# Performance work log

Hardware: AMD Instinct MI355X
Metric: run time of the kernel (lower is better)

The kernel has to match this reference:

```python
import jax, jax.numpy as jnp
import numpy as np

B, S, HID, H = 8, 128, 256, 4
DH = HID // H
FF = 4 * HID


def setup_inputs() -> dict:
    key = jax.random.key(0)
    ks = jax.random.split(key, 16)
    n = lambda i, shape: jax.random.normal(ks[i], shape, dtype=jnp.float32) * 0.02
    z = lambda shape: jnp.zeros(shape, dtype=jnp.float32)
    return dict(
        x=jax.random.normal(ks[0], (B, S, HID), dtype=jnp.float32),
        attention_mask=jnp.zeros((B, 1, S, S), dtype=jnp.float32),
        Wq=n(1, (HID, HID)), bq=z((HID,)),
        Wk=n(2, (HID, HID)), bk=z((HID,)),
        Wv=n(3, (HID, HID)), bv=z((HID,)),
        order_w=n(4, (2 * DH,)), order_b=z(()),
        dist_w=n(5, (2 * DH,)), dist_b=z(()),
        scalar=jax.random.normal(ks[6], (1,), dtype=jnp.float32),
        AWq=n(7, (HID, HID)), Abq=z((HID,)),
        AWk=n(8, (HID, HID)), Abk=z((HID,)),
        Wd=n(9, (HID, HID)), bd=z((HID,)),
        g1=jnp.ones((HID,), jnp.float32), beta1=z((HID,)),
        W1=n(10, (HID, FF)), b1=z((FF,)),
        W2=n(11, (FF, HID)), b2=z((HID,)),
        g2=jnp.ones((HID,), jnp.float32), beta2=z((HID,)),
    )


def _ln(t, g, b, eps=1e-12):
    m = t.mean(-1, keepdims=True)
    v = ((t - m) ** 2).mean(-1, keepdims=True)
    return (t - m) / jnp.sqrt(v + eps) * g + b


def _heads(t):
    # [B,S,HID] -> [B,H,S,DH]
    return t.reshape(B, S, H, DH).transpose(0, 2, 1, 3)


def reference(x, attention_mask, Wq, bq, Wk, bk, Wv, bv, order_w, order_b,
              dist_w, dist_b, scalar, AWq, Abq, AWk, Abk, Wd, bd,
              g1, beta1, W1, b1, W2, b2, g2, beta2):
    inv = 1.0 / jnp.sqrt(jnp.float32(DH))
    q = x @ Wq + bq
    k = x @ Wk + bk
    v = x @ Wv + bv
    qh, kh, vh = _heads(q), _heads(k), _heads(v)
    scores = jnp.einsum('bhqd,bhkd->bhqk', qh, kh)  # [B,H,S,S]

    # order/distance affines on concat(q_i, k_j): Linear(2*DH,1) decomposes into
    # per-token projections summed via broadcast (same math, no [B,H,S,S,2*DH] tensor)
    pr_order = jax.nn.sigmoid((qh @ order_w[:DH])[..., :, None]
                              + (kh @ order_w[DH:])[..., None, :] + order_b)
    gd_order = jnp.triu(jnp.ones((S, S), jnp.float32), k=1)
    err_order = (jnp.log(pr_order + 1e-24) * gd_order
                 + jnp.log(1.0 - pr_order + 1e-24) * (1.0 - gd_order))

    idx = jnp.arange(S)
    gd_dist = jnp.log(jnp.abs(idx[None, :] - idx[:, None]).astype(jnp.float32) + 1.0)
    pr_dist = ((qh @ dist_w[:DH])[..., :, None]
               + (kh @ dist_w[DH:])[..., None, :] + dist_b)
    err_dist = -jnp.square(gd_dist - pr_dist) * jnp.square(scalar[0]) * 0.5

    rich_scores = scores + err_order + err_dist
    softm = lambda s: jax.nn.softmax(s * inv + attention_mask, axis=-1)
    rich_probs = softm(rich_scores)
    origin_probs = softm(scores)

    # rich/calibrated combine ('fixed'): softmax(origin + 0.5 * rich)
    combined = jax.nn.softmax(origin_probs + 0.5 * rich_probs, axis=-1)

    # two-level attack attention on transformed mixed q/k
    aq, ak = _heads(q @ AWq + Abq), _heads(k @ AWk + Abk)
    attack_probs = softm(jnp.einsum('bhqd,bhkd->bhqk', aq, ak))
    final_probs = jax.nn.softmax(combined + 0.5 * attack_probs, axis=-1)

    ctx = jnp.einsum('bhqk,bhkd->bhqd', final_probs, vh)
    ctx = ctx.transpose(0, 2, 1, 3).reshape(B, S, HID)
    h = _ln(ctx @ Wd + bd + x, g1, beta1)
    f = jax.nn.gelu(h @ W1 + b1, approximate=False) @ W2 + b2
    return _ln(f + h, g2, beta2)
```

## Files before the change

### kernel.cpp

```cpp
#include <hip/hip_runtime.h>
#include <hip/hip_bf16.h>
#include <math.h>

#define B_  8
#define S_  128
#define HID_ 256
#define H_  4
#define DH_ 64
#define FF_ 1024
#define M_  (B_ * S_)

typedef _Float16 half_t;
typedef __attribute__((ext_vector_type(8))) _Float16 half8;
typedef __attribute__((ext_vector_type(4))) float floatx4;

enum { EP_F32 = 0, EP_F16 = 1, EP_F16B = 2, EP_GELU = 3, EP_PROJ = 4 };

__device__ __forceinline__ floatx4 mfma16(half8 a, half8 b, floatx4 c) {
    return __builtin_amdgcn_mfma_f32_16x16x32_f16(a, b, c, 0, 0, 0);
}

__device__ __forceinline__ float wred_sum(float v) {
#pragma unroll
    for (int o = 32; o >= 1; o >>= 1) v += __shfl_xor(v, o, 64);
    return v;
}
__device__ __forceinline__ float block_sum_256(float v, float* s4, int tid) {
    v = wred_sum(v);
    __syncthreads();
    if ((tid & 63) == 0) s4[tid >> 6] = v;
    __syncthreads();
    return s4[0] + s4[1] + s4[2] + s4[3];
}
__device__ __forceinline__ float qred_sum(float v) {
#pragma unroll
    for (int o = 1; o < 16; o <<= 1) v += __shfl_xor(v, o, 64);
    return v;
}
__device__ __forceinline__ void sm8(float (&v)[8]) {
    float s = 0.f;
#pragma unroll
    for (int j = 0; j < 8; ++j) { v[j] = __expf(v[j]); s += v[j]; }
    s = qred_sum(s);
    float r = 1.f / s;
#pragma unroll
    for (int j = 0; j < 8; ++j) v[j] *= r;
}

template<int EPI>
__device__ __forceinline__ void mgemm(
    const half_t* __restrict__ A, int ldA,
    const half_t* __restrict__ Bt, int ldB,
    int kLen, int m0, int n0,
    const float* __restrict__ bias,
    float* __restrict__ Cf, half_t* __restrict__ Ch, int ldC,
    const float* __restrict__ pw1, const float* __restrict__ pw2,
    float* __restrict__ po1, float* __restrict__ po2, int hsel)
{
    __shared__ half8 Asf[2][4][64];
    __shared__ half8 Bsf[2][4][64];

    const int tid = threadIdx.x;
    const int w = tid >> 6, l = tid & 63;
    const int sr = tid >> 2;
    const int sq = tid & 3;
    const int sdst = (sr & 15) | (sq << 4);
    const int smt = sr >> 4;
    const half_t* Ap = A + (size_t)(m0 + sr) * ldA + sq * 8;
    const half_t* Bp = Bt + (size_t)(n0 + sr) * ldB + sq * 8;

    half8 ra, rb;
    auto fetch = [&](int t) {
        ra = *(const half8*)(Ap + t * 32);
        rb = *(const half8*)(Bp + t * 32);
    };
    auto commit = [&](int buf) {
        Asf[buf][smt][sdst] = ra;
        Bsf[buf][smt][sdst] = rb;
    };

    floatx4 zero = {0.f, 0.f, 0.f, 0.f};
    floatx4 acc[4] = {zero, zero, zero, zero};
    const int kt = kLen >> 5;

    fetch(0);
    commit(0);
    __syncthreads();
    for (int t = 0; t < kt; ++t) {
        const bool more = (t + 1 < kt);
        if (more) fetch(t + 1);
        const int buf = t & 1;
        half8 a = Asf[buf][w][l];
        acc[0] = mfma16(a, Bsf[buf][0][l], acc[0]);
        acc[1] = mfma16(a, Bsf[buf][1][l], acc[1]);
        acc[2] = mfma16(a, Bsf[buf][2][l], acc[2]);
        acc[3] = mfma16(a, Bsf[buf][3][l], acc[3]);
        if (more) {
            commit((t + 1) & 1);
            __syncthreads();
        }
    }

    const int quad = l >> 4, lc = l & 15;
    const int rowb = m0 + w * 16 + quad * 4;
    float bvv[4] = {0.f, 0.f, 0.f, 0.f};
    if (EPI >= EP_F16B) {
#pragma unroll
        for (int nt = 0; nt < 4; ++nt) bvv[nt] = bias[n0 + nt * 16 + lc];
    }
    float pw1v[4], pw2v[4];
    if (EPI == EP_PROJ) {
#pragma unroll
        for (int nt = 0; nt < 4; ++nt) {
            pw1v[nt] = pw1[nt * 16 + lc];
            pw2v[nt] = pw2[nt * 16 + lc];
        }
    }
#pragma unroll
    for (int rr = 0; rr < 4; ++rr) {
        float ov[4];
#pragma unroll
        for (int nt = 0; nt < 4; ++nt) {
            float o = acc[nt][rr];
            if (EPI >= EP_F16B) o += bvv[nt];
            if (EPI == EP_GELU) o = 0.5f * o * (1.f + erff(o * 0.70710678118654752f));
            ov[nt] = o;
            const size_t ci = (size_t)(rowb + rr) * ldC + n0 + nt * 16 + lc;
            if (EPI == EP_F32) Cf[ci] = o;
            else Ch[ci] = (half_t)o;
        }
        if (EPI == EP_PROJ) {
            float po = ov[0] * pw1v[0] + ov[1] * pw1v[1] + ov[2] * pw1v[2] + ov[3] * pw1v[3];
            float pd = ov[0] * pw2v[0] + ov[1] * pw2v[1] + ov[2] * pw2v[2] + ov[3] * pw2v[3];
#pragma unroll
            for (int off = 1; off < 16; off <<= 1) {
                po += __shfl_xor(po, off, 64);
                pd += __shfl_xor(pd, off, 64);
            }
            if (lc == 0) {
                const int m = rowb + rr;
                const int idx = ((m >> 7) * H_ + hsel) * S_ + (m & 127);
                po1[idx] = po;
                po2[idx] = pd;
            }
        }
    }
}

__global__ __launch_bounds__(256) void prep_kernel(
    const float* __restrict__ x,
    const float* __restrict__ Wq, const float* __restrict__ Wk,
    const float* __restrict__ Wv, const float* __restrict__ Wd,
    const float* __restrict__ AWq, const float* __restrict__ AWk,
    const float* __restrict__ W1, const float* __restrict__ W2,
    half_t* __restrict__ x16, half_t* __restrict__ Wq16n, half_t* __restrict__ Wk16n,
    half_t* __restrict__ WqT, half_t* __restrict__ WkT, half_t* __restrict__ WvT,
    half_t* __restrict__ WdT, half_t* __restrict__ AWqT, half_t* __restrict__ AWkT,
    half_t* __restrict__ W1T, half_t* __restrict__ W2T)
{
    const int z = blockIdx.z, bx = blockIdx.x, by = blockIdx.y;
    const int tid = threadIdx.x;
    if (z < 3) {
        const float* src = (z == 0) ? x : (z == 1) ? Wq : Wk;
        half_t* dst = (z == 0) ? x16 : (z == 1) ? Wq16n : Wk16n;
        const int total = (z == 0) ? M_ * HID_ : HID_ * HID_;
        const int bid = by * 16 + bx;
        if (bid * 1024 < total) {
            const int base = bid * 1024 + tid * 4;
            float4 vv = *(const float4*)(src + base);
            dst[base + 0] = (half_t)vv.x;
            dst[base + 1] = (half_t)vv.y;
            dst[base + 2] = (half_t)vv.z;
            dst[base + 3] = (half_t)vv.w;
        }
        return;
    }
    const float* src; half_t* dst; int K, N, k0, n0;
    if (z <= 8) {
        const float* ins[6] = {Wq, Wk, Wv, Wd, AWq, AWk};
        half_t* outs[6] = {WqT, WkT, WvT, WdT, AWqT, AWkT};
        src = ins[z - 3]; dst = outs[z - 3];
        K = 256; N = 256; k0 = bx * 64; n0 = by * 64;
        if (bx >= 4 || by >= 4) return;
    } else if (z == 9) {
        src = W1; dst = W1T; K = 256; N = 1024;
        k0 = bx * 64; n0 = by * 64;
        if (bx >= 4) return;
    } else {
        src = W2; dst = W2T; K = 1024; N = 256;
        k0 = by * 64; n0 = bx * 64;
        if (bx >= 4) return;
    }
    __shared__ half_t tl[64][72];
    const int r = tid >> 2, c0 = (tid & 3) * 16;
#pragma unroll 4
    for (int i = 0; i < 16; ++i)
        tl[c0 + i][r] = (half_t)src[(size_t)(k0 + r) * N + n0 + c0 + i];
    __syncthreads();
#pragma unroll 4
    for (int i = 0; i < 16; ++i)
        dst[(size_t)(n0 + r) * K + k0 + c0 + i] = tl[r][c0 + i];
}

__global__ __launch_bounds__(256) void compose_mfma(
    const half_t* __restrict__ AWqT, const half_t* __restrict__ AWkT,
    const half_t* __restrict__ Wq16n, const half_t* __restrict__ Wk16n,
    const float* __restrict__ AWq, const float* __restrict__ AWk,
    const float* __restrict__ bq, const float* __restrict__ bk,
    const float* __restrict__ Abq, const float* __restrict__ Abk,
    half_t* __restrict__ WcqT, half_t* __restrict__ WckT,
    float* __restrict__ bcq, float* __restrict__ bck)
{
    const int z = blockIdx.z;
    if (blockIdx.y < 4) {
        const half_t* A = z ? AWkT : AWqT;
        const half_t* Bt = z ? Wk16n : Wq16n;
        half_t* C = z ? WckT : WcqT;
        mgemm<EP_F16>(A, HID_, Bt, HID_, HID_, blockIdx.y * 64, blockIdx.x * 64,
                      nullptr, nullptr, C, HID_, nullptr, nullptr, nullptr, nullptr, 0);
    } else {
        __shared__ float red[4][64];
        const float* bsrc = z ? bk : bq;
        const float* AW   = z ? AWk : AWq;
        const float* Ab   = z ? Abk : Abq;
        float* bco        = z ? bck : bcq;
        int t = threadIdx.x, l = t & 63, kc = t >> 6;
        int n = blockIdx.x * 64 + l;
        float p = 0.f;
#pragma unroll 8
        for (int kk = 0; kk < 64; ++kk) {
            int k = kc * 64 + kk;
            p = fmaf(bsrc[k], AW[(size_t)k * HID_ + n], p);
        }
        red[kc][l] = p;
        __syncthreads();
        if (kc == 0)
            bco[n] = red[0][l] + red[1][l] + red[2][l] + red[3][l] + Ab[n];
    }
}

__global__ __launch_bounds__(256) void xgemm5(
    const half_t* __restrict__ x16,
    const half_t* __restrict__ WqT, const float* __restrict__ bq,
    const half_t* __restrict__ WkT, const float* __restrict__ bk,
    const half_t* __restrict__ WvT, const float* __restrict__ bv,
    const half_t* __restrict__ WcqT, const float* __restrict__ bcq,
    const half_t* __restrict__ WckT, const float* __restrict__ bck,
    const float* __restrict__ order_w, const float* __restrict__ dist_w,
    half_t* __restrict__ q16, half_t* __restrict__ k16, half_t* __restrict__ v16,
    half_t* __restrict__ aq16, half_t* __restrict__ ak16,
    float* __restrict__ qoA, float* __restrict__ qdA,
    float* __restrict__ koA, float* __restrict__ kdA)
{
    const int z = blockIdx.z;
    const int m0 = blockIdx.y * 64, n0 = blockIdx.x * 64;
    if (z == 0)
        mgemm<EP_PROJ>(x16, HID_, WqT, HID_, HID_, m0, n0, bq, nullptr, q16, HID_,
                       order_w, dist_w, qoA, qdA, blockIdx.x);
    else if (z == 1)
        mgemm<EP_PROJ>(x16, HID_, WkT, HID_, HID_, m0, n0, bk, nullptr, k16, HID_,
                       order_w + DH_, dist_w + DH_, koA, kdA, blockIdx.x);
    else if (z == 2)
        mgemm<EP_F16B>(x16, HID_, WvT, HID_, HID_, m0, n0, bv, nullptr, v16, HID_,
                       nullptr, nullptr, nullptr, nullptr, 0);
    else if (z == 3)
        mgemm<EP_F16B>(x16, HID_, WcqT, HID_, HID_, m0, n0, bcq, nullptr, aq16, HID_,
                       nullptr, nullptr, nullptr, nullptr, 0);
    else
        mgemm<EP_F16B>(x16, HID_, WckT, HID_, HID_, m0, n0, bck, nullptr, ak16, HID_,
                       nullptr, nullptr, nullptr, nullptr, 0);
}

__global__ __launch_bounds__(64) void attn_fused(
    const half_t* __restrict__ q16, const half_t* __restrict__ k16,
    const half_t* __restrict__ v16, const half_t* __restrict__ aq16,
    const half_t* __restrict__ ak16,
    const float* __restrict__ qoA, const float* __restrict__ qdA,
    const float* __restrict__ koA, const float* __restrict__ kdA,
    const float* __restrict__ mask,
    const float* __restrict__ order_b_p, const float* __restrict__ dist_b_p,
    const float* __restrict__ scalar_p,
    half_t* __restrict__ ctx16)
{
    __shared__ half8 Qf[2][64], AQf[2][64];
    __shared__ half8 Kf[2][8][64], AKf[2][8][64];
    __shared__ half_t Vt[64][136];
    __shared__ half_t Pm[16][136];

    const int l = threadIdx.x;
    const int quad = l >> 4, lc = l & 15;
    const int bh = blockIdx.x >> 3, rt = blockIdx.x & 7;
    const int b = bh >> 2, h = bh & 3;
    const size_t hoff = (size_t)b * S_ * HID_ + h * DH_;

#pragma unroll
    for (int u = 0; u < 2; ++u) {
        int idx = u * 64 + l;
        int r = idx >> 3, c = idx & 7;
        size_t g = hoff + (size_t)(rt * 16 + r) * HID_ + c * 8;
        int kt = c >> 2, sl = r | ((c & 3) << 4);
        Qf[kt][sl]  = *(const half8*)(q16 + g);
        AQf[kt][sl] = *(const half8*)(aq16 + g);
    }
#pragma unroll
    for (int u = 0; u < 16; ++u) {
        int idx = u * 64 + l;
        int j = idx >> 3, c = idx & 7;
        size_t g = hoff + (size_t)j * HID_ + c * 8;
        int kt = c >> 2, jt = j >> 4, sl = (j & 15) | ((c & 3) << 4);
        Kf[kt][jt][sl]  = *(const half8*)(k16 + g);
        AKf[kt][jt][sl] = *(const half8*)(ak16 + g);
    }
#pragma unroll
    for (int u = 0; u < 16; ++u) {
        int j = (u >> 3) * 64 + l;
        int c = u & 7;
        half8 vv = *(const half8*)(v16 + hoff + (size_t)j * HID_ + c * 8);
#pragma unroll
        for (int e = 0; e < 8; ++e) Vt[c * 8 + e][j] = vv[e];
    }
    __syncthreads();

    floatx4 zero = {0.f, 0.f, 0.f, 0.f};
    floatx4 accS[8], accA[8];
#pragma unroll
    for (int jt = 0; jt < 8; ++jt) { accS[jt] = zero; accA[jt] = zero; }
#pragma unroll
    for (int kt = 0; kt < 2; ++kt) {
        half8 a0 = Qf[kt][l];
        half8 a1 = AQf[kt][l];
#pragma unroll
        for (int jt = 0; jt < 8; ++jt) {
            accS[jt] = mfma16(a0, Kf[kt][jt][l], accS[jt]);
            accA[jt] = mfma16(a1, AKf[kt][jt][l], accA[jt]);
        }
    }

    const float ob = order_b_p[0], db = dist_b_p[0];
    const float scl = scalar_p[0];
    const float s2 = scl * scl;
    const float inv = 0.125f;
    float kov[8], kdv[8];
#pragma unroll
    for (int jt = 0; jt < 8; ++jt) {
        kov[jt] = koA[bh * S_ + jt * 16 + lc];
        kdv[jt] = kdA[bh * S_ + jt * 16 + lc];
    }
#pragma unroll
    for (int reg = 0; reg < 4; ++reg) {
        const int il = quad * 4 + reg;
        const int i  = rt * 16 + il;
        float qo = qoA[bh * S_ + i], qd = qdA[bh * S_ + i];
        const float* mrow = mask + ((size_t)(b * S_ + i)) * S_;
        float mk[8], lg[8], as_[8];
#pragma unroll
        for (int jt = 0; jt < 8; ++jt) {
            mk[jt] = mrow[jt * 16 + lc];
            lg[jt] = accS[jt][reg];
            as_[jt] = accA[jt][reg];
        }
        float p0[8];
#pragma unroll
        for (int jt = 0; jt < 8; ++jt) p0[jt] = lg[jt] * inv + mk[jt];
        sm8(p0);
        float p1[8];
#pragma unroll
        for (int jt = 0; jt < 8; ++jt) {
            int j = jt * 16 + lc;
            float pr = 1.f / (1.f + __expf(-(qo + kov[jt] + ob)));
            float sel = (j > i) ? pr : 1.f - pr;
            float erro = __logf(sel + 1e-24f);
            float gd = __logf(fabsf((float)(j - i)) + 1.f);
            float dd = gd - (qd + kdv[jt] + db);
            p1[jt] = (lg[jt] + erro - 0.5f * dd * dd * s2) * inv + mk[jt];
        }
        sm8(p1);
#pragma unroll
        for (int jt = 0; jt < 8; ++jt) p0[jt] += 0.5f * p1[jt];
        sm8(p0);
#pragma unroll
        for (int jt = 0; jt < 8; ++jt) p1[jt] = as_[jt] * inv + mk[jt];
        sm8(p1);
#pragma unroll
        for (int jt = 0; jt < 8; ++jt) p0[jt] += 0.5f * p1[jt];
        sm8(p0);
#pragma unroll
        for (int jt = 0; jt < 8; ++jt) Pm[il][jt * 16 + lc] = (half_t)p0[jt];
    }
    __syncthreads();

    half8 pa_[4];
#pragma unroll
    for (int kt = 0; kt < 4; ++kt)
        pa_[kt] = *(const half8*)&Pm[lc][kt * 32 + quad * 8];
    floatx4 apv[4];
#pragma unroll
    for (int nt = 0; nt < 4; ++nt) apv[nt] = zero;
#pragma unroll
    for (int nt = 0; nt < 4; ++nt) {
#pragma unroll
        for (int kt = 0; kt < 4; ++kt) {
            half8 vf = *(const half8*)&Vt[nt * 16 + lc][kt * 32 + quad * 8];
            apv[nt] = mfma16(pa_[kt], vf, apv[nt]);
        }
    }
#pragma unroll
    for (int nt = 0; nt < 4; ++nt) {
#pragma unroll
        for (int reg = 0; reg < 4; ++reg) {
            int i = rt * 16 + quad * 4 + reg;
            ctx16[hoff + (size_t)i * HID_ + nt * 16 + lc] = (half_t)apv[nt][reg];
        }
    }
}

__global__ __launch_bounds__(256) void dense_mfma(
    const half_t* __restrict__ ctx16, const half_t* __restrict__ WdT,
    float* __restrict__ dn)
{
    mgemm<EP_F32>(ctx16, HID_, WdT, HID_, HID_, blockIdx.y * 64, blockIdx.x * 64,
                  nullptr, dn, nullptr, HID_, nullptr, nullptr, nullptr, nullptr, 0);
}

__global__ __launch_bounds__(256) void ff1_mfma(
    const half_t* __restrict__ h16, const half_t* __restrict__ W1T,
    const float* __restrict__ b1, half_t* __restrict__ f116)
{
    mgemm<EP_GELU>(h16, HID_, W1T, HID_, HID_, blockIdx.y * 64, blockIdx.x * 64,
                   b1, nullptr, f116, FF_, nullptr, nullptr, nullptr, nullptr, 0);
}

__global__ __launch_bounds__(256) void ff2_mfma(
    const half_t* __restrict__ f116, const half_t* __restrict__ W2T,
    float* __restrict__ p0, float* __restrict__ p1,
    float* __restrict__ p2, float* __restrict__ p3)
{
    const int z = blockIdx.z;
    float* C = (z == 0) ? p0 : (z == 1) ? p1 : (z == 2) ? p2 : p3;
    mgemm<EP_F32>(f116 + z * 256, FF_, W2T + z * 256, FF_, 256,
                  blockIdx.y * 64, blockIdx.x * 64,
                  nullptr, C, nullptr, HID_, nullptr, nullptr, nullptr, nullptr, 0);
}

__global__ __launch_bounds__(256) void ln1_kernel(
    const float* __restrict__ dn, const float* __restrict__ bd,
    const float* __restrict__ x,
    const float* __restrict__ g1, const float* __restrict__ beta1,
    float* __restrict__ h32, half_t* __restrict__ h16)
{
    __shared__ float s4[4];
    const int row = blockIdx.x;
    const int n = threadIdx.x;
    const size_t idx = (size_t)row * HID_ + n;
    float val = dn[idx] + bd[n] + x[idx];
    float mean = block_sum_256(val, s4, n) * (1.f / HID_);
    float dv = val - mean;
    float var = block_sum_256(dv * dv, s4, n) * (1.f / HID_);
    float r = dv * rsqrtf(var + 1e-12f) * g1[n] + beta1[n];
    h32[idx] = r;
    h16[idx] = (half_t)r;
}

__global__ __launch_bounds__(256) void ln2_kernel(
    const float* __restrict__ p0, const float* __restrict__ p1,
    const float* __restrict__ p2, const float* __restrict__ p3,
    const float* __restrict__ b2, const float* __restrict__ h32,
    const float* __restrict__ g2, const float* __restrict__ beta2,
    float* __restrict__ out)
{
    __shared__ float s4[4];
    const int row = blockIdx.x;
    const int n = threadIdx.x;
    const size_t idx = (size_t)row * HID_ + n;
    float val = p0[idx] + p1[idx] + p2[idx] + p3[idx] + b2[n] + h32[idx];
    float mean = block_sum_256(val, s4, n) * (1.f / HID_);
    float dv = val - mean;
    float var = block_sum_256(dv * dv, s4, n) * (1.f / HID_);
    out[idx] = dv * rsqrtf(var + 1e-12f) * g2[n] + beta2[n];
}

extern "C" void kernel_launch(void* const* d_in, const int* in_sizes, int n_in,
                              void* d_out, int out_size, void* d_ws, size_t ws_size,
                              hipStream_t stream) {
    const float* x        = (const float*)d_in[0];
    const float* mask     = (const float*)d_in[1];
    const float* Wq       = (const float*)d_in[2];
    const float* bq       = (const float*)d_in[3];
    const float* Wk       = (const float*)d_in[4];
    const float* bk       = (const float*)d_in[5];
    const float* Wv       = (const float*)d_in[6];
    const float* bv       = (const float*)d_in[7];
    const float* order_w  = (const float*)d_in[8];
    const float* order_b  = (const float*)d_in[9];
    const float* dist_w   = (const float*)d_in[10];
    const float* dist_b   = (const float*)d_in[11];
    const float* scalar   = (const float*)d_in[12];
    const float* AWq      = (const float*)d_in[13];
    const float* Abq      = (const float*)d_in[14];
    const float* AWk      = (const float*)d_in[15];
    const float* Abk      = (const float*)d_in[16];
    const float* Wd       = (const float*)d_in[17];
    const float* bd       = (const float*)d_in[18];
    const float* g1       = (const float*)d_in[19];
    const float* beta1    = (const float*)d_in[20];
    const float* W1       = (const float*)d_in[21];
    const float* b1       = (const float*)d_in[22];
    const float* W2       = (const float*)d_in[23];
    const float* b2       = (const float*)d_in[24];
    const float* g2       = (const float*)d_in[25];
    const float* beta2    = (const float*)d_in[26];

    float* ws = (float*)d_ws;
    size_t off = 0;
    auto afl = [&](size_t n) { float* p = ws + off; off += n; return p; };
    auto ahf = [&](size_t nh) { half_t* p = (half_t*)(ws + off); off += nh / 2; return p; };

    half_t* x16   = ahf(M_ * HID_);
    half_t* Wq16n = ahf(HID_ * HID_);
    half_t* Wk16n = ahf(HID_ * HID_);
    half_t* WqT   = ahf(HID_ * HID_);
    half_t* WkT   = ahf(HID_ * HID_);
    half_t* WvT   = ahf(HID_ * HID_);
    half_t* WdT   = ahf(HID_ * HID_);
    half_t* AWqT  = ahf(HID_ * HID_);
    half_t* AWkT  = ahf(HID_ * HID_);
    half_t* W1T   = ahf(HID_ * FF_);
    half_t* W2T   = ahf(HID_ * FF_);
    half_t* WcqT  = ahf(HID_ * HID_);
    half_t* WckT  = ahf(HID_ * HID_);
    half_t* q16   = ahf(M_ * HID_);
    half_t* k16   = ahf(M_ * HID_);
    half_t* v16   = ahf(M_ * HID_);
    half_t* aq16  = ahf(M_ * HID_);
    half_t* ak16  = ahf(M_ * HID_);
    half_t* ctx16 = ahf(M_ * HID_);
    half_t* h16   = ahf(M_ * HID_);
    half_t* f116  = ahf(M_ * FF_);
    float* dnb  = afl(M_ * HID_);
    float* hb32 = afl(M_ * HID_);
    float* pf0  = afl(M_ * HID_);
    float* pf1  = afl(M_ * HID_);
    float* pf2  = afl(M_ * HID_);
    float* pf3  = afl(M_ * HID_);
    float* bcq  = afl(256);
    float* bck  = afl(256);
    float* qoA  = afl(B_ * H_ * S_);
    float* qdA  = afl(B_ * H_ * S_);
    float* koA  = afl(B_ * H_ * S_);
    float* kdA  = afl(B_ * H_ * S_);

    prep_kernel<<<dim3(16, 16, 11), 256, 0, stream>>>(
        x, Wq, Wk, Wv, Wd, AWq, AWk, W1, W2,
        x16, Wq16n, Wk16n, WqT, WkT, WvT, WdT, AWqT, AWkT, W1T, W2T);
    compose_mfma<<<dim3(4, 5, 2), 256, 0, stream>>>(
        AWqT, AWkT, Wq16n, Wk16n, AWq, AWk, bq, bk, Abq, Abk, WcqT, WckT, bcq, bck);
    xgemm5<<<dim3(4, 16, 5), 256, 0, stream>>>(
        x16, WqT, bq, WkT, bk, WvT, bv, WcqT, bcq, WckT, bck, order_w, dist_w,
        q16, k16, v16, aq16, ak16, qoA, qdA, koA, kdA);
    attn_fused<<<256, 64, 0, stream>>>(
        q16, k16, v16, aq16, ak16, qoA, qdA, koA, kdA,
        mask, order_b, dist_b, scalar, ctx16);
    dense_mfma<<<dim3(4, 16), 256, 0, stream>>>(ctx16, WdT, dnb);
    ln1_kernel<<<M_, 256, 0, stream>>>(dnb, bd, x, g1, beta1, hb32, h16);
    ff1_mfma<<<dim3(16, 16), 256, 0, stream>>>(h16, W1T, b1, f116);
    ff2_mfma<<<dim3(4, 16, 4), 256, 0, stream>>>(f116, W2T, pf0, pf1, pf2, pf3);
    ln2_kernel<<<M_, 256, 0, stream>>>(pf0, pf1, pf2, pf3, b2, hb32, g2, beta2, (float*)d_out);
}
```

Measured before the change: 162.4 us.

## Merge all stages into one cooperative persistent kernel with grid syncs

Result: slower. 432.5 us (+166.3%).

```diff
diff --git a/kernel.cpp b/kernel.cpp
--- a/kernel.cpp
+++ b/kernel.cpp
@@ -1,6 +1,8 @@
 #include <hip/hip_runtime.h>
-#include <hip/hip_bf16.h>
+#include <hip/hip_cooperative_groups.h>
 #include <math.h>
+
+namespace cg = cooperative_groups;
 
 #define B_  8
 #define S_  128
@@ -25,13 +27,6 @@
     for (int o = 32; o >= 1; o >>= 1) v += __shfl_xor(v, o, 64);
     return v;
 }
-__device__ __forceinline__ float block_sum_256(float v, float* s4, int tid) {
-    v = wred_sum(v);
-    __syncthreads();
-    if ((tid & 63) == 0) s4[tid >> 6] = v;
-    __syncthreads();
-    return s4[0] + s4[1] + s4[2] + s4[3];
-}
 __device__ __forceinline__ float qred_sum(float v) {
 #pragma unroll
     for (int o = 1; o < 16; o <<= 1) v += __shfl_xor(v, o, 64);
@@ -49,6 +44,7 @@
 
 template<int EPI>
 __device__ __forceinline__ void mgemm(
+    half8* __restrict__ Asf, half8* __restrict__ Bsf,
     const half_t* __restrict__ A, int ldA,
     const half_t* __restrict__ Bt, int ldB,
     int kLen, int m0, int n0,
@@ -57,9 +53,6 @@
     const float* __restrict__ pw1, const float* __restrict__ pw2,
     float* __restrict__ po1, float* __restrict__ po2, int hsel)
 {
-    __shared__ half8 Asf[2][4][64];
-    __shared__ half8 Bsf[2][4][64];
-
     const int tid = threadIdx.x;
     const int w = tid >> 6, l = tid & 63;
     const int sr = tid >> 2;
@@ -75,8 +68,8 @@
         rb = *(const half8*)(Bp + t * 32);
     };
     auto commit = [&](int buf) {
-        Asf[buf][smt][sdst] = ra;
-        Bsf[buf][smt][sdst] = rb;
+        Asf[(buf * 4 + smt) * 64 + sdst] = ra;
+        Bsf[(buf * 4 + smt) * 64 + sdst] = rb;
     };
 
     floatx4 zero = {0.f, 0.f, 0.f, 0.f};
@@ -90,11 +83,11 @@
         const bool more = (t + 1 < kt);
         if (more) fetch(t + 1);
         const int buf = t & 1;
-        half8 a = Asf[buf][w][l];
-        acc[0] = mfma16(a, Bsf[buf][0][l], acc[0]);
-        acc[1] = mfma16(a, Bsf[buf][1][l], acc[1]);
-        acc[2] = mfma16(a, Bsf[buf][2][l], acc[2]);
-        acc[3] = mfma16(a, Bsf[buf][3][l], acc[3]);
+        half8 a = Asf[(buf * 4 + w) * 64 + l];
+        acc[0] = mfma16(a, Bsf[(buf * 4 + 0) * 64 + l], acc[0]);
+        acc[1] = mfma16(a, Bsf[(buf * 4 + 1) * 64 + l], acc[1]);
+        acc[2] = mfma16(a, Bsf[(buf * 4 + 2) * 64 + l], acc[2]);
+        acc[3] = mfma16(a, Bsf[(buf * 4 + 3) * 64 + l], acc[3]);
         if (more) {
             commit((t + 1) & 1);
             __syncthreads();
@@ -147,422 +140,412 @@
     }
 }
 
-__global__ __launch_bounds__(256) void prep_kernel(
-    const float* __restrict__ x,
-    const float* __restrict__ Wq, const float* __restrict__ Wk,
-    const float* __restrict__ Wv, const float* __restrict__ Wd,
-    const float* __restrict__ AWq, const float* __restrict__ AWk,
-    const float* __restrict__ W1, const float* __restrict__ W2,
-    half_t* __restrict__ x16, half_t* __restrict__ Wq16n, half_t* __restrict__ Wk16n,
-    half_t* __restrict__ WqT, half_t* __restrict__ WkT, half_t* __restrict__ WvT,
-    half_t* __restrict__ WdT, half_t* __restrict__ AWqT, half_t* __restrict__ AWkT,
-    half_t* __restrict__ W1T, half_t* __restrict__ W2T)
-{
-    const int z = blockIdx.z, bx = blockIdx.x, by = blockIdx.y;
+struct MonoArgs {
+    const float *x, *mask;
+    const float *Wq, *bq, *Wk, *bk, *Wv, *bv;
+    const float *order_w, *order_b, *dist_w, *dist_b, *scalar;
+    const float *AWq, *Abq, *AWk, *Abk;
+    const float *Wd, *bd, *g1, *beta1, *W1, *b1, *W2, *b2, *g2, *beta2;
+    half_t *x16, *Wq16n, *Wk16n, *WqT, *WkT, *WvT, *WdT, *AWqT, *AWkT, *W1T, *W2T;
+    half_t *WcqT, *WckT;
+    half_t *q16, *k16, *v16, *aq16, *ak16, *ctx16, *h16, *f116;
+    float *dnb, *hb32, *pf0, *pf1, *pf2, *pf3;
+    float *bcq, *bck, *qoA, *qdA, *koA, *kdA;
+    float *out;
+};
+
+__global__ __launch_bounds__(256) void mono(MonoArgs a) {
+    cg::grid_group grid = cg::this_grid();
+    __shared__ __align__(16) char smem[58624];
+
+    const int bid = blockIdx.x;
     const int tid = threadIdx.x;
-    if (z < 3) {
-        const float* src = (z == 0) ? x : (z == 1) ? Wq : Wk;
-        half_t* dst = (z == 0) ? x16 : (z == 1) ? Wq16n : Wk16n;
-        const int total = (z == 0) ? M_ * HID_ : HID_ * HID_;
-        const int bid = by * 16 + bx;
-        if (bid * 1024 < total) {
-            const int base = bid * 1024 + tid * 4;
-            float4 vv = *(const float4*)(src + base);
-            dst[base + 0] = (half_t)vv.x;
-            dst[base + 1] = (half_t)vv.y;
-            dst[base + 2] = (half_t)vv.z;
-            dst[base + 3] = (half_t)vv.w;
-        }
-        return;
-    }
-    const float* src; half_t* dst; int K, N, k0, n0;
-    if (z <= 8) {
-        const float* ins[6] = {Wq, Wk, Wv, Wd, AWq, AWk};
-        half_t* outs[6] = {WqT, WkT, WvT, WdT, AWqT, AWkT};
-        src = ins[z - 3]; dst = outs[z - 3];
-        K = 256; N = 256; k0 = bx * 64; n0 = by * 64;
-        if (bx >= 4 || by >= 4) return;
-    } else if (z == 9) {
-        src = W1; dst = W1T; K = 256; N = 1024;
-        k0 = bx * 64; n0 = by * 64;
-        if (bx >= 4) return;
+    const int w = tid >> 6, l = tid & 63;
+    const int quad = l >> 4, lc = l & 15;
+
+    if (bid < 224) {
+        const float* src; half_t* dst; int K, N, k0, n0;
+        if (bid < 96) {
+            const float* ins[6] = {a.Wq, a.Wk, a.Wv, a.Wd, a.AWq, a.AWk};
+            half_t* outs[6] = {a.WqT, a.WkT, a.WvT, a.WdT, a.AWqT, a.AWkT};
+            src = ins[bid >> 4]; dst = outs[bid >> 4];
+            int tt = bid & 15;
+            K = 256; N = 256; k0 = (tt & 3) * 64; n0 = (tt >> 2) * 64;
+        } else if (bid < 160) {
+            int tt = bid - 96;
+            src = a.W1; dst = a.W1T; K = 256; N = 1024;
+            k0 = (tt & 3) * 64; n0 = (tt >> 2) * 64;
+        } else {
+            int tt = bid - 160;
+            src = a.W2; dst = a.W2T; K = 1024; N = 256;
+            k0 = (tt >> 2) * 64; n0 = (tt & 3) * 64;
+        }
+        half_t* tl = (half_t*)smem;
+        const int r = tid >> 2, c0 = (tid & 3) * 16;
+#pragma unroll 4
+        for (int i = 0; i < 16; ++i)
+            tl[(size_t)(c0 + i) * 72 + r] = (half_t)src[(size_t)(k0 + r) * N + n0 + c0 + i];
+        __syncthreads();
+#pragma unroll 4
+        for (int i = 0; i < 16; ++i)
+            dst[(size_t)(n0 + r) * K + k0 + c0 + i] = tl[(size_t)r * 72 + c0 + i];
     } else {
-        src = W2; dst = W2T; K = 1024; N = 256;
-        k0 = by * 64; n0 = bx * 64;
-        if (bx >= 4) return;
-    }
-    __shared__ half_t tl[64][72];
-    const int r = tid >> 2, c0 = (tid & 3) * 16;
-#pragma unroll 4
-    for (int i = 0; i < 16; ++i)
-        tl[c0 + i][r] = (half_t)src[(size_t)(k0 + r) * N + n0 + c0 + i];
-    __syncthreads();
-#pragma unroll 4
-    for (int i = 0; i < 16; ++i)
-        dst[(size_t)(n0 + r) * K + k0 + c0 + i] = tl[r][c0 + i];
-}
-
-__global__ __launch_bounds__(256) void compose_mfma(
-    const half_t* __restrict__ AWqT, const half_t* __restrict__ AWkT,
-    const half_t* __restrict__ Wq16n, const half_t* __restrict__ Wk16n,
-    const float* __restrict__ AWq, const float* __restrict__ AWk,
-    const float* __restrict__ bq, const float* __restrict__ bk,
-    const float* __restrict__ Abq, const float* __restrict__ Abk,
-    half_t* __restrict__ WcqT, half_t* __restrict__ WckT,
-    float* __restrict__ bcq, float* __restrict__ bck)
-{
-    const int z = blockIdx.z;
-    if (blockIdx.y < 4) {
-        const half_t* A = z ? AWkT : AWqT;
-        const half_t* Bt = z ? Wk16n : Wq16n;
-        half_t* C = z ? WckT : WcqT;
-        mgemm<EP_F16>(A, HID_, Bt, HID_, HID_, blockIdx.y * 64, blockIdx.x * 64,
+        const int base = (bid - 224) * 12288;
+#pragma unroll
+        for (int it = 0; it < 12; ++it) {
+            int gi = base + it * 1024 + tid * 4;
+            const float* s; half_t* d; int o;
+            if (gi < 262144)      { s = a.x;  d = a.x16;   o = gi; }
+            else if (gi < 327680) { s = a.Wq; d = a.Wq16n; o = gi - 262144; }
+            else                  { s = a.Wk; d = a.Wk16n; o = gi - 327680; }
+            float4 vv = *(const float4*)(s + o);
+            d[o + 0] = (half_t)vv.x;
+            d[o + 1] = (half_t)vv.y;
+            d[o + 2] = (half_t)vv.z;
+            d[o + 3] = (half_t)vv.w;
+        }
+    }
+    grid.sync();
+
+    if (bid < 32) {
+        const int z = bid >> 4;
+        const int tt = bid & 15;
+        const half_t* A  = z ? a.AWkT : a.AWqT;
+        const half_t* Bt = z ? a.Wk16n : a.Wq16n;
+        half_t* C = z ? a.WckT : a.WcqT;
+        mgemm<EP_F16>((half8*)smem, (half8*)(smem + 8192),
+                      A, HID_, Bt, HID_, HID_, (tt >> 2) * 64, (tt & 3) * 64,
                       nullptr, nullptr, C, HID_, nullptr, nullptr, nullptr, nullptr, 0);
-    } else {
-        __shared__ float red[4][64];
-        const float* bsrc = z ? bk : bq;
-        const float* AW   = z ? AWk : AWq;
-        const float* Ab   = z ? Abk : Abq;
-        float* bco        = z ? bck : bcq;
-        int t = threadIdx.x, l = t & 63, kc = t >> 6;
-        int n = blockIdx.x * 64 + l;
+    } else if (bid < 34) {
+        const int z = bid - 32;
+        const float* bsrc = z ? a.bk : a.bq;
+        const float* AW   = z ? a.AWk : a.AWq;
+        const float* Ab   = z ? a.Abk : a.Abq;
+        float* bco        = z ? a.bck : a.bcq;
         float p = 0.f;
 #pragma unroll 8
-        for (int kk = 0; kk < 64; ++kk) {
-            int k = kc * 64 + kk;
-            p = fmaf(bsrc[k], AW[(size_t)k * HID_ + n], p);
-        }
-        red[kc][l] = p;
+        for (int k = 0; k < 256; ++k)
+            p = fmaf(bsrc[k], AW[(size_t)k * HID_ + tid], p);
+        bco[tid] = p + Ab[tid];
+    }
+    grid.sync();
+
+    for (int t = bid; t < 320; t += 256) {
+        const int z = t >> 6;
+        const int tt = t & 63;
+        const int m0 = (tt >> 2) * 64, n0 = (tt & 3) * 64;
+        half8* As = (half8*)smem; half8* Bs = (half8*)(smem + 8192);
+        if (z == 0)
+            mgemm<EP_PROJ>(As, Bs, a.x16, HID_, a.WqT, HID_, HID_, m0, n0,
+                           a.bq, nullptr, a.q16, HID_,
+                           a.order_w, a.dist_w, a.qoA, a.qdA, tt & 3);
+        else if (z == 1)
+            mgemm<EP_PROJ>(As, Bs, a.x16, HID_, a.WkT, HID_, HID_, m0, n0,
+                           a.bk, nullptr, a.k16, HID_,
+                           a.order_w + DH_, a.dist_w + DH_, a.koA, a.kdA, tt & 3);
+        else if (z == 2)
+            mgemm<EP_F16B>(As, Bs, a.x16, HID_, a.WvT, HID_, HID_, m0, n0,
+                           a.bv, nullptr, a.v16, HID_, nullptr, nullptr, nullptr, nullptr, 0);
+        else if (z == 3)
+            mgemm<EP_F16B>(As, Bs, a.x16, HID_, a.WcqT, HID_, HID_, m0, n0,
+                           a.bcq, nullptr, a.aq16, HID_, nullptr, nullptr, nullptr, nullptr, 0);
+        else
+            mgemm<EP_F16B>(As, Bs, a.x16, HID_, a.WckT, HID_, HID_, m0, n0,
+                           a.bck, nullptr, a.ak16, HID_, nullptr, nullptr, nullptr, nullptr, 0);
+        if (t + 256 < 320) __syncthreads();
+    }
+    grid.sync();
+
+    {
+        half8* Qf  = (half8*)smem;
+        half8* AQf = (half8*)(smem + 2048);
+        half8* Kf  = (half8*)(smem + 4096);
+        half8* AKf = (half8*)(smem + 20480);
+        half_t* Vt = (half_t*)(smem + 36864);
+        half_t* Pm = (half_t*)(smem + 54272);
+
+        const int bh = bid >> 3, rt = bid & 7;
+        const int b = bh >> 2, h = bh & 3;
+        const size_t hoff = (size_t)b * S_ * HID_ + h * DH_;
+
+        if (tid < 128) {
+            int r = tid >> 3, c = tid & 7;
+            size_t g = hoff + (size_t)(rt * 16 + r) * HID_ + c * 8;
+            int kt = c >> 2, sl = r | ((c & 3) << 4);
+            Qf[kt * 64 + sl]  = *(const half8*)(a.q16 + g);
+            AQf[kt * 64 + sl] = *(const half8*)(a.aq16 + g);
+        }
+#pragma unroll
+        for (int u = 0; u < 4; ++u) {
+            int idx = u * 256 + tid;
+            int j = idx >> 3, c = idx & 7;
+            size_t g = hoff + (size_t)j * HID_ + c * 8;
+            int kt = c >> 2, jt = j >> 4, sl = (j & 15) | ((c & 3) << 4);
+            Kf[(kt * 8 + jt) * 64 + sl]  = *(const half8*)(a.k16 + g);
+            AKf[(kt * 8 + jt) * 64 + sl] = *(const half8*)(a.ak16 + g);
+        }
+#pragma unroll
+        for (int u = 0; u < 4; ++u) {
+            int idx = u * 256 + tid;
+            int c = idx >> 7, j = idx & 127;
+            half8 vv = *(const half8*)(a.v16 + hoff + (size_t)j * HID_ + c * 8);
+#pragma unroll
+            for (int e = 0; e < 8; ++e) Vt[(size_t)(c * 8 + e) * 136 + j] = vv[e];
+        }
         __syncthreads();
-        if (kc == 0)
-            bco[n] = red[0][l] + red[1][l] + red[2][l] + red[3][l] + Ab[n];
-    }
-}
-
-__global__ __launch_bounds__(256) void xgemm5(
-    const half_t* __restrict__ x16,
-    const half_t* __restrict__ WqT, const float* __restrict__ bq,
-    const half_t* __restrict__ WkT, const float* __restrict__ bk,
-    const half_t* __restrict__ WvT, const float* __restrict__ bv,
-    const half_t* __restrict__ WcqT, const float* __restrict__ bcq,
-    const half_t* __restrict__ WckT, const float* __restrict__ bck,
-    const float* __restrict__ order_w, const float* __restrict__ dist_w,
-    half_t* __restrict__ q16, half_t* __restrict__ k16, half_t* __restrict__ v16,
-    half_t* __restrict__ aq16, half_t* __restrict__ ak16,
-    float* __restrict__ qoA, float* __restrict__ qdA,
-    float* __restrict__ koA, float* __restrict__ kdA)
-{
-    const int z = blockIdx.z;
-    const int m0 = blockIdx.y * 64, n0 = blockIdx.x * 64;
-    if (z == 0)
-        mgemm<EP_PROJ>(x16, HID_, WqT, HID_, HID_, m0, n0, bq, nullptr, q16, HID_,
-                       order_w, dist_w, qoA, qdA, blockIdx.x);
-    else if (z == 1)
-        mgemm<EP_PROJ>(x16, HID_, WkT, HID_, HID_, m0, n0, bk, nullptr, k16, HID_,
-                       order_w + DH_, dist_w + DH_, koA, kdA, blockIdx.x);
-    else if (z == 2)
-        mgemm<EP_F16B>(x16, HID_, WvT, HID_, HID_, m0, n0, bv, nullptr, v16, HID_,
-                       nullptr, nullptr, nullptr, nullptr, 0);
-    else if (z == 3)
-        mgemm<EP_F16B>(x16, HID_, WcqT, HID_, HID_, m0, n0, bcq, nullptr, aq16, HID_,
-                       nullptr, nullptr, nullptr, nullptr, 0);
-    else
-        mgemm<EP_F16B>(x16, HID_, WckT, HID_, HID_, m0, n0, bck, nullptr, ak16, HID_,
-                       nullptr, nullptr, nullptr, nullptr, 0);
-}
-
-__global__ __launch_bounds__(64) void attn_fused(
-    const half_t* __restrict__ q16, const half_t* __restrict__ k16,
-    const half_t* __restrict__ v16, const half_t* __restrict__ aq16,
-    const half_t* __restrict__ ak16,
-    const float* __restrict__ qoA, const float* __restrict__ qdA,
-    const float* __restrict__ koA, const float* __restrict__ kdA,
-    const float* __restrict__ mask,
-    const float* __restrict__ order_b_p, const float* __restrict__ dist_b_p,
-    const float* __restrict__ scalar_p,
-    half_t* __restrict__ ctx16)
-{
-    __shared__ half8 Qf[2][64], AQf[2][64];
-    __shared__ half8 Kf[2][8][64], AKf[2][8][64];
-    __shared__ half_t Vt[64][136];
-    __shared__ half_t Pm[16][136];
-
-    const int l = threadIdx.x;
-    const int quad = l >> 4, lc = l & 15;
-    const int bh = blockIdx.x >> 3, rt = blockIdx.x & 7;
-    const int b = bh >> 2, h = bh & 3;
-    const size_t hoff = (size_t)b * S_ * HID_ + h * DH_;
-
-#pragma unroll
-    for (int u = 0; u < 2; ++u) {
-        int idx = u * 64 + l;
-        int r = idx >> 3, c = idx & 7;
-        size_t g = hoff + (size_t)(rt * 16 + r) * HID_ + c * 8;
-        int kt = c >> 2, sl = r | ((c & 3) << 4);
-        Qf[kt][sl]  = *(const half8*)(q16 + g);
-        AQf[kt][sl] = *(const half8*)(aq16 + g);
-    }
-#pragma unroll
-    for (int u = 0; u < 16; ++u) {
-        int idx = u * 64 + l;
-        int j = idx >> 3, c = idx & 7;
-        size_t g = hoff + (size_t)j * HID_ + c * 8;
-        int kt = c >> 2, jt = j >> 4, sl = (j & 15) | ((c & 3) << 4);
-        Kf[kt][jt][sl]  = *(const half8*)(k16 + g);
-        AKf[kt][jt][sl] = *(const half8*)(ak16 + g);
-    }
-#pragma unroll
-    for (int u = 0; u < 16; ++u) {
-        int j = (u >> 3) * 64 + l;
-        int c = u & 7;
-        half8 vv = *(const half8*)(v16 + hoff + (size_t)j * HID_ + c * 8);
-#pragma unroll
-        for (int e = 0; e < 8; ++e) Vt[c * 8 + e][j] = vv[e];
-    }
-    __syncthreads();
-
-    floatx4 zero = {0.f, 0.f, 0.f, 0.f};
-    floatx4 accS[8], accA[8];
-#pragma unroll
-    for (int jt = 0; jt < 8; ++jt) { accS[jt] = zero; accA[jt] = zero; }
-#pragma unroll
-    for (int kt = 0; kt < 2; ++kt) {
-        half8 a0 = Qf[kt][l];
-        half8 a1 = AQf[kt][l];
-#pragma unroll
-        for (int jt = 0; jt < 8; ++jt) {
-            accS[jt] = mfma16(a0, Kf[kt][jt][l], accS[jt]);
-            accA[jt] = mfma16(a1, AKf[kt][jt][l], accA[jt]);
-        }
-    }
-
-    const float ob = order_b_p[0], db = dist_b_p[0];
-    const float scl = scalar_p[0];
-    const float s2 = scl * scl;
-    const float inv = 0.125f;
-    float kov[8], kdv[8];
-#pragma unroll
-    for (int jt = 0; jt < 8; ++jt) {
-        kov[jt] = koA[bh * S_ + jt * 16 + lc];
-        kdv[jt] = kdA[bh * S_ + jt * 16 + lc];
-    }
-#pragma unroll
-    for (int reg = 0; reg < 4; ++reg) {
-        const int il = quad * 4 + reg;
-        const int i  = rt * 16 + il;
-        float qo = qoA[bh * S_ + i], qd = qdA[bh * S_ + i];
-        const float* mrow = mask + ((size_t)(b * S_ + i)) * S_;
-        float mk[8], lg[8], as_[8];
-#pragma unroll
-        for (int jt = 0; jt < 8; ++jt) {
-            mk[jt] = mrow[jt * 16 + lc];
-            lg[jt] = accS[jt][reg];
-            as_[jt] = accA[jt][reg];
-        }
-        float p0[8];
-#pragma unroll
-        for (int jt = 0; jt < 8; ++jt) p0[jt] = lg[jt] * inv + mk[jt];
-        sm8(p0);
-        float p1[8];
-#pragma unroll
-        for (int jt = 0; jt < 8; ++jt) {
-            int j = jt * 16 + lc;
-            float pr = 1.f / (1.f + __expf(-(qo + kov[jt] + ob)));
-            float sel = (j > i) ? pr : 1.f - pr;
-            float erro = __logf(sel + 1e-24f);
-            float gd = __logf(fabsf((float)(j - i)) + 1.f);
-            float dd = gd - (qd + kdv[jt] + db);
-            p1[jt] = (lg[jt] + erro - 0.5f * dd * dd * s2) * inv + mk[jt];
-        }
-        sm8(p1);
-#pragma unroll
-        for (int jt = 0; jt < 8; ++jt) p0[jt] += 0.5f * p1[jt];
-        sm8(p0);
-#pragma unroll
-        for (int jt = 0; jt < 8; ++jt) p1[jt] = as_[jt] * inv + mk[jt];
-        sm8(p1);
-#pragma unroll
-        for (int jt = 0; jt < 8; ++jt) p0[jt] += 0.5f * p1[jt];
-        sm8(p0);
-#pragma unroll
-        for (int jt = 0; jt < 8; ++jt) Pm[il][jt * 16 + lc] = (half_t)p0[jt];
-    }
-    __syncthreads();
-
-    half8 pa_[4];
-#pragma unroll
-    for (int kt = 0; kt < 4; ++kt)
-        pa_[kt] = *(const half8*)&Pm[lc][kt * 32 + quad * 8];
-    floatx4 apv[4];
-#pragma unroll
-    for (int nt = 0; nt < 4; ++nt) apv[nt] = zero;
-#pragma unroll
-    for (int nt = 0; nt < 4; ++nt) {
-#pragma unroll
-        for (int kt = 0; kt < 4; ++kt) {
-            half8 vf = *(const half8*)&Vt[nt * 16 + lc][kt * 32 + quad * 8];
-            apv[nt] = mfma16(pa_[kt], vf, apv[nt]);
-        }
-    }
-#pragma unroll
-    for (int nt = 0; nt < 4; ++nt) {
-#pragma unroll
-        for (int reg = 0; reg < 4; ++reg) {
-            int i = rt * 16 + quad * 4 + reg;
-            ctx16[hoff + (size_t)i * HID_ + nt * 16 + lc] = (half_t)apv[nt][reg];
-        }
-    }
-}
-
-__global__ __launch_bounds__(256) void dense_mfma(
-    const half_t* __restrict__ ctx16, const half_t* __restrict__ WdT,
-    float* __restrict__ dn)
-{
-    mgemm<EP_F32>(ctx16, HID_, WdT, HID_, HID_, blockIdx.y * 64, blockIdx.x * 64,
-                  nullptr, dn, nullptr, HID_, nullptr, nullptr, nullptr, nullptr, 0);
-}
-
-__global__ __launch_bounds__(256) void ff1_mfma(
-    const half_t* __restrict__ h16, const half_t* __restrict__ W1T,
-    const float* __restrict__ b1, half_t* __restrict__ f116)
-{
-    mgemm<EP_GELU>(h16, HID_, W1T, HID_, HID_, blockIdx.y * 64, blockIdx.x * 64,
-                   b1, nullptr, f116, FF_, nullptr, nullptr, nullptr, nullptr, 0);
-}
-
-__global__ __launch_bounds__(256) void ff2_mfma(
-    const half_t* __restrict__ f116, const half_t* __restrict__ W2T,
-    float* __restrict__ p0, float* __restrict__ p1,
-    float* __restrict__ p2, float* __restrict__ p3)
-{
-    const int z = blockIdx.z;
-    float* C = (z == 0) ? p0 : (z == 1) ? p1 : (z == 2) ? p2 : p3;
-    mgemm<EP_F32>(f116 + z * 256, FF_, W2T + z * 256, FF_, 256,
-                  blockIdx.y * 64, blockIdx.x * 64,
-                  nullptr, C, nullptr, HID_, nullptr, nullptr, nullptr, nullptr, 0);
-}
-
-__global__ __launch_bounds__(256) void ln1_kernel(
-    const float* __restrict__ dn, const float* __restrict__ bd,
-    const float* __restrict__ x,
-    const float* __restrict__ g1, const float* __restrict__ beta1,
-    float* __restrict__ h32, half_t* __restrict__ h16)
-{
-    __shared__ float s4[4];
-    const int row = blockIdx.x;
-    const int n = threadIdx.x;
-    const size_t idx = (size_t)row * HID_ + n;
-    float val = dn[idx] + bd[n] + x[idx];
-    float mean = block_sum_256(val, s4, n) * (1.f / HID_);
-    float dv = val - mean;
-    float var = block_sum_256(dv * dv, s4, n) * (1.f / HID_);
-    float r = dv * rsqrtf(var + 1e-12f) * g1[n] + beta1[n];
-    h32[idx] = r;
-    h16[idx] = (half_t)r;
-}
-
-__global__ __launch_bounds__(256) void ln2_kernel(
-    const float* __restrict__ p0, const float* __restrict__ p1,
-    const float* __restrict__ p2, const float* __restrict__ p3,
-    const float* __restrict__ b2, const float* __restrict__ h32,
-    const float* __restrict__ g2, const float* __restrict__ beta2,
-    float* __restrict__ out)
-{
-    __shared__ float s4[4];
-    const int row = blockIdx.x;
-    const int n = threadIdx.x;
-    const size_t idx = (size_t)row * HID_ + n;
-    float val = p0[idx] + p1[idx] + p2[idx] + p3[idx] + b2[n] + h32[idx];
-    float mean = block_sum_256(val, s4, n) * (1.f / HID_);
-    float dv = val - mean;
-    float var = block_sum_256(dv * dv, s4, n) * (1.f / HID_);
-    out[idx] = dv * rsqrtf(var + 1e-12f) * g2[n] + beta2[n];
+
+        if (tid < 64) {
+            floatx4 zero = {0.f, 0.f, 0.f, 0.f};
+            floatx4 accS[8], accA[8];
+#pragma unroll
+            for (int jt = 0; jt < 8; ++jt) { accS[jt] = zero; accA[jt] = zero; }
+#pragma unroll
+            for (int kt = 0; kt < 2; ++kt) {
+                half8 a0 = Qf[kt * 64 + l];
+                half8 a1 = AQf[kt * 64 + l];
+#pragma unroll
+                for (int jt = 0; jt < 8; ++jt) {
+                    accS[jt] = mfma16(a0, Kf[(kt * 8 + jt) * 64 + l], accS[jt]);
+                    accA[jt] = mfma16(a1, AKf[(kt * 8 + jt) * 64 + l], accA[jt]);
+                }
+            }
+
+            const float ob = a.order_b[0], db = a.dist_b[0];
+            const float scl = a.scalar[0];
+            const float s2 = scl * scl;
+            const float inv = 0.125f;
+            float kov[8], kdv[8];
+#pragma unroll
+            for (int jt = 0; jt < 8; ++jt) {
+                kov[jt] = a.koA[bh * S_ + jt * 16 + lc];
+                kdv[jt] = a.kdA[bh * S_ + jt * 16 + lc];
+            }
+#pragma unroll
+            for (int reg = 0; reg < 4; ++reg) {
+                const int il = quad * 4 + reg;
+                const int i  = rt * 16 + il;
+                float qo = a.qoA[bh * S_ + i], qd = a.qdA[bh * S_ + i];
+                const float* mrow = a.mask + ((size_t)(b * S_ + i)) * S_;
+                float mk[8], lg[8], as_[8];
+#pragma unroll
+                for (int jt = 0; jt < 8; ++jt) {
+                    mk[jt] = mrow[jt * 16 + lc];
+                    lg[jt] = accS[jt][reg];
+                    as_[jt] = accA[jt][reg];
+                }
+                float p0[8];
+#pragma unroll
+                for (int jt = 0; jt < 8; ++jt) p0[jt] = lg[jt] * inv + mk[jt];
+                sm8(p0);
+                float p1[8];
+#pragma unroll
+                for (int jt = 0; jt < 8; ++jt) {
+                    int j = jt * 16 + lc;
+                    float pr = 1.f / (1.f + __expf(-(qo + kov[jt] + ob)));
+                    float sel = (j > i) ? pr : 1.f - pr;
+                    float erro = __logf(sel + 1e-24f);
+                    float gd = __logf(fabsf((float)(j - i)) + 1.f);
+                    float dd = gd - (qd + kdv[jt] + db);
+                    p1[jt] = (lg[jt] + erro - 0.5f * dd * dd * s2) * inv + mk[jt];
+                }
+                sm8(p1);
+#pragma unroll
+                for (int jt = 0; jt < 8; ++jt) p0[jt] += 0.5f * p1[jt];
+                sm8(p0);
+#pragma unroll
+                for (int jt = 0; jt < 8; ++jt) p1[jt] = as_[jt] * inv + mk[jt];
+                sm8(p1);
+#pragma unroll
+                for (int jt = 0; jt < 8; ++jt) p0[jt] += 0.5f * p1[jt];
+                sm8(p0);
+#pragma unroll
+                for (int jt = 0; jt < 8; ++jt) Pm[(size_t)il * 136 + jt * 16 + lc] = (half_t)p0[jt];
+            }
+            half8 pa_[4];
+#pragma unroll
+            for (int kt = 0; kt < 4; ++kt)
+                pa_[kt] = *(const half8*)&Pm[(size_t)lc * 136 + kt * 32 + quad * 8];
+            floatx4 apv[4];
+#pragma unroll
+            for (int nt = 0; nt < 4; ++nt) apv[nt] = zero;
+#pragma unroll
+            for (int nt = 0; nt < 4; ++nt) {
+#pragma unroll
+                for (int kt = 0; kt < 4; ++kt) {
+                    half8 vf = *(const half8*)&Vt[(size_t)(nt * 16 + lc) * 136 + kt * 32 + quad * 8];
+                    apv[nt] = mfma16(pa_[kt], vf, apv[nt]);
+                }
+            }
+#pragma unroll
+            for (int nt = 0; nt < 4; ++nt) {
+#pragma unroll
+                for (int reg = 0; reg < 4; ++reg) {
+                    int i = rt * 16 + quad * 4 + reg;
+                    a.ctx16[hoff + (size_t)i * HID_ + nt * 16 + lc] = (half_t)apv[nt][reg];
+                }
+            }
+        }
+    }
+    grid.sync();
+
+    if (bid < 64) {
+        mgemm<EP_F32>((half8*)smem, (half8*)(smem + 8192),
+                      a.ctx16, HID_, a.WdT, HID_, HID_,
+                      (bid >> 2) * 64, (bid & 3) * 64,
+                      nullptr, a.dnb, nullptr, HID_, nullptr, nullptr, nullptr, nullptr, 0);
+    }
+    grid.sync();
+
+    {
+        const int row = bid * 4 + w;
+        const size_t ro = (size_t)row * HID_ + l * 4;
+        float4 dv4 = *(const float4*)(a.dnb + ro);
+        float4 bd4 = *(const float4*)(a.bd + l * 4);
+        float4 x4  = *(const float4*)(a.x + ro);
+        float v0 = dv4.x + bd4.x + x4.x;
+        float v1 = dv4.y + bd4.y + x4.y;
+        float v2 = dv4.z + bd4.z + x4.z;
+        float v3 = dv4.w + bd4.w + x4.w;
+        float s = wred_sum(v0 + v1 + v2 + v3);
+        float mean = s * (1.f / HID_);
+        v0 -= mean; v1 -= mean; v2 -= mean; v3 -= mean;
+        float sq = wred_sum(v0 * v0 + v1 * v1 + v2 * v2 + v3 * v3);
+        float rstd = rsqrtf(sq * (1.f / HID_) + 1e-12f);
+        float4 g4 = *(const float4*)(a.g1 + l * 4);
+        float4 be4 = *(const float4*)(a.beta1 + l * 4);
+        float4 o;
+        o.x = v0 * rstd * g4.x + be4.x;
+        o.y = v1 * rstd * g4.y + be4.y;
+        o.z = v2 * rstd * g4.z + be4.z;
+        o.w = v3 * rstd * g4.w + be4.w;
+        *(float4*)(a.hb32 + ro) = o;
+        a.h16[ro + 0] = (half_t)o.x;
+        a.h16[ro + 1] = (half_t)o.y;
+        a.h16[ro + 2] = (half_t)o.z;
+        a.h16[ro + 3] = (half_t)o.w;
+    }
+    grid.sync();
+
+    {
+        const int m0 = (bid >> 4) * 64, n0 = (bid & 15) * 64;
+        mgemm<EP_GELU>((half8*)smem, (half8*)(smem + 8192),
+                       a.h16, HID_, a.W1T, HID_, HID_, m0, n0,
+                       a.b1, nullptr, a.f116, FF_, nullptr, nullptr, nullptr, nullptr, 0);
+    }
+    grid.sync();
+
+    {
+        const int z = bid >> 6;
+        const int tt = bid & 63;
+        float* C = (z == 0) ? a.pf0 : (z == 1) ? a.pf1 : (z == 2) ? a.pf2 : a.pf3;
+        mgemm<EP_F32>((half8*)smem, (half8*)(smem + 8192),
+                      a.f116 + z * 256, FF_, a.W2T + z * 256, FF_, 256,
+                      (tt >> 2) * 64, (tt & 3) * 64,
+                      nullptr, C, nullptr, HID_, nullptr, nullptr, nullptr, nullptr, 0);
+    }
+    grid.sync();
+
+    {
+        const int row = bid * 4 + w;
+        const size_t ro = (size_t)row * HID_ + l * 4;
+        float4 p04 = *(const float4*)(a.pf0 + ro);
+        float4 p14 = *(const float4*)(a.pf1 + ro);
+        float4 p24 = *(const float4*)(a.pf2 + ro);
+        float4 p34 = *(const float4*)(a.pf3 + ro);
+        float4 b24 = *(const float4*)(a.b2 + l * 4);
+        float4 h4  = *(const float4*)(a.hb32 + ro);
+        float v0 = p04.x + p14.x + p24.x + p34.x + b24.x + h4.x;
+        float v1 = p04.y + p14.y + p24.y + p34.y + b24.y + h4.y;
+        float v2 = p04.z + p14.z + p24.z + p34.z + b24.z + h4.z;
+        float v3 = p04.w + p14.w + p24.w + p34.w + b24.w + h4.w;
+        float s = wred_sum(v0 + v1 + v2 + v3);
+        float mean = s * (1.f / HID_);
+        v0 -= mean; v1 -= mean; v2 -= mean; v3 -= mean;
+        float sq = wred_sum(v0 * v0 + v1 * v1 + v2 * v2 + v3 * v3);
+        float rstd = rsqrtf(sq * (1.f / HID_) + 1e-12f);
+        float4 g4 = *(const float4*)(a.g2 + l * 4);
+        float4 be4 = *(const float4*)(a.beta2 + l * 4);
+        float4 o;
+        o.x = v0 * rstd * g4.x + be4.x;
+        o.y = v1 * rstd * g4.y + be4.y;
+        o.z = v2 * rstd * g4.z + be4.z;
+        o.w = v3 * rstd * g4.w + be4.w;
+        *(float4*)(a.out + ro) = o;
+    }
 }
 
 extern "C" void kernel_launch(void* const* d_in, const int* in_sizes, int n_in,
                               void* d_out, int out_size, void* d_ws, size_t ws_size,
                               hipStream_t stream) {
-    const float* x        = (const float*)d_in[0];
-    const float* mask     = (const float*)d_in[1];
-    const float* Wq       = (const float*)d_in[2];
-    const float* bq       = (const float*)d_in[3];
-    const float* Wk       = (const float*)d_in[4];
-    const float* bk       = (const float*)d_in[5];
-    const float* Wv       = (const float*)d_in[6];
-    const float* bv       = (const float*)d_in[7];
-    const float* order_w  = (const float*)d_in[8];
-    const float* order_b  = (const float*)d_in[9];
-    const float* dist_w   = (const float*)d_in[10];
-    const float* dist_b   = (const float*)d_in[11];
-    const float* scalar   = (const float*)d_in[12];
-    const float* AWq      = (const float*)d_in[13];
-    const float* Abq      = (const float*)d_in[14];
-    const float* AWk      = (const float*)d_in[15];
-    const float* Abk      = (const float*)d_in[16];
-    const float* Wd       = (const float*)d_in[17];
-    const float* bd       = (const float*)d_in[18];
-    const float* g1       = (const float*)d_in[19];
-    const float* beta1    = (const float*)d_in[20];
-    const float* W1       = (const float*)d_in[21];
-    const float* b1       = (const float*)d_in[22];
-    const float* W2       = (const float*)d_in[23];
-    const float* b2       = (const float*)d_in[24];
-    const float* g2       = (const float*)d_in[25];
-    const float* beta2    = (const float*)d_in[26];
+    MonoArgs a;
+    a.x        = (const float*)d_in[0];
+    a.mask     = (const float*)d_in[1];
+    a.Wq       = (const float*)d_in[2];
+    a.bq       = (const float*)d_in[3];
+    a.Wk       = (const float*)d_in[4];
+    a.bk       = (const float*)d_in[5];
+    a.Wv       = (const float*)d_in[6];
+    a.bv       = (const float*)d_in[7];
+    a.order_w  = (const float*)d_in[8];
+    a.order_b  = (const float*)d_in[9];
+    a.dist_w   = (const float*)d_in[10];
+    a.dist_b   = (const float*)d_in[11];
+    a.scalar   = (const float*)d_in[12];
+    a.AWq      = (const float*)d_in[13];
+    a.Abq      = (const float*)d_in[14];
+    a.AWk      = (const float*)d_in[15];
+    a.Abk      = (const float*)d_in[16];
+    a.Wd       = (const float*)d_in[17];
+    a.bd       = (const float*)d_in[18];
+    a.g1       = (const float*)d_in[19];
+    a.beta1    = (const float*)d_in[20];
+    a.W1       = (const float*)d_in[21];
+    a.b1       = (const float*)d_in[22];
+    a.W2       = (const float*)d_in[23];
+    a.b2       = (const float*)d_in[24];
+    a.g2       = (const float*)d_in[25];
+    a.beta2    = (const float*)d_in[26];
 
     float* ws = (float*)d_ws;
     size_t off = 0;
     auto afl = [&](size_t n) { float* p = ws + off; off += n; return p; };
     auto ahf = [&](size_t nh) { half_t* p = (half_t*)(ws + off); off += nh / 2; return p; };
 
-    half_t* x16   = ahf(M_ * HID_);
-    half_t* Wq16n = ahf(HID_ * HID_);
-    half_t* Wk16n = ahf(HID_ * HID_);
-    half_t* WqT   = ahf(HID_ * HID_);
-    half_t* WkT   = ahf(HID_ * HID_);
-    half_t* WvT   = ahf(HID_ * HID_);
-    half_t* WdT   = ahf(HID_ * HID_);
-    half_t* AWqT  = ahf(HID_ * HID_);
-    half_t* AWkT  = ahf(HID_ * HID_);
-    half_t* W1T   = ahf(HID_ * FF_);
-    half_t* W2T   = ahf(HID_ * FF_);
-    half_t* WcqT  = ahf(HID_ * HID_);
-    half_t* WckT  = ahf(HID_ * HID_);
-    half_t* q16   = ahf(M_ * HID_);
-    half_t* k16   = ahf(M_ * HID_);
-    half_t* v16   = ahf(M_ * HID_);
-    half_t* aq16  = ahf(M_ * HID_);
-    half_t* ak16  = ahf(M_ * HID_);
-    half_t* ctx16 = ahf(M_ * HID_);
-    half_t* h16   = ahf(M_ * HID_);
-    half_t* f116  = ahf(M_ * FF_);
-    float* dnb  = afl(M_ * HID_);
-    float* hb32 = afl(M_ * HID_);
-    float* pf0  = afl(M_ * HID_);
-    float* pf1  = afl(M_ * HID_);
-    float* pf2  = afl(M_ * HID_);
-    float* pf3  = afl(M_ * HID_);
-    float* bcq  = afl(256);
-    float* bck  = afl(256);
-    float* qoA  = afl(B_ * H_ * S_);
-    float* qdA  = afl(B_ * H_ * S_);
-    float* koA  = afl(B_ * H_ * S_);
-    float* kdA  = afl(B_ * H_ * S_);
-
-    prep_kernel<<<dim3(16, 16, 11), 256, 0, stream>>>(
-        x, Wq, Wk, Wv, Wd, AWq, AWk, W1, W2,
-        x16, Wq16n, Wk16n, WqT, WkT, WvT, WdT, AWqT, AWkT, W1T, W2T);
-    compose_mfma<<<dim3(4, 5, 2), 256, 0, stream>>>(
-        AWqT, AWkT, Wq16n, Wk16n, AWq, AWk, bq, bk, Abq, Abk, WcqT, WckT, bcq, bck);
-    xgemm5<<<dim3(4, 16, 5), 256, 0, stream>>>(
-        x16, WqT, bq, WkT, bk, WvT, bv, WcqT, bcq, WckT, bck, order_w, dist_w,
-        q16, k16, v16, aq16, ak16, qoA, qdA, koA, kdA);
-    attn_fused<<<256, 64, 0, stream>>>(
-        q16, k16, v16, aq16, ak16, qoA, qdA, koA, kdA,
-        mask, order_b, dist_b, scalar, ctx16);
-    dense_mfma<<<dim3(4, 16), 256, 0, stream>>>(ctx16, WdT, dnb);
-    ln1_kernel<<<M_, 256, 0, stream>>>(dnb, bd, x, g1, beta1, hb32, h16);
-    ff1_mfma<<<dim3(16, 16), 256, 0, stream>>>(h16, W1T, b1, f116);
-    ff2_mfma<<<dim3(4, 16, 4), 256, 0, stream>>>(f116, W2T, pf0, pf1, pf2, pf3);
-    ln2_kernel<<<M_, 256, 0, stream>>>(pf0, pf1, pf2, pf3, b2, hb32, g2, beta2, (float*)d_out);
-}
+    a.x16   = ahf(M_ * HID_);
+    a.Wq16n = ahf(HID_ * HID_);
+    a.Wk16n = ahf(HID_ * HID_);
+    a.WqT   = ahf(HID_ * HID_);
+    a.WkT   = ahf(HID_ * HID_);
+    a.WvT   = ahf(HID_ * HID_);
+    a.WdT   = ahf(HID_ * HID_);
+    a.AWqT  = ahf(HID_ * HID_);
+    a.AWkT  = ahf(HID_ * HID_);
+    a.W1T   = ahf(HID_ * FF_);
+    a.W2T   = ahf(HID_ * FF_);
+    a.WcqT  = ahf(HID_ * HID_);
+    a.WckT  = ahf(HID_ * HID_);
+    a.q16   = ahf(M_ * HID_);
+    a.k16   = ahf(M_ * HID_);
+    a.v16   = ahf(M_ * HID_);
+    a.aq16  = ahf(M_ * HID_);
+    a.ak16  = ahf(M_ * HID_);
+    a.ctx16 = ahf(M_ * HID_);
+    a.h16   = ahf(M_ * HID_);
+    a.f116  = ahf(M_ * FF_);
+    a.dnb  = afl(M_ * HID_);
+    a.hb32 = afl(M_ * HID_);
+    a.pf0  = afl(M_ * HID_);
+    a.pf1  = afl(M_ * HID_);
+    a.pf2  = afl(M_ * HID_);
+    a.pf3  = afl(M_ * HID_);
+    a.bcq  = afl(256);
+    a.bck  = afl(256);
+    a.qoA  = afl(B_ * H_ * S_);
+    a.qdA  = afl(B_ * H_ * S_);
+    a.koA  = afl(B_ * H_ * S_);
+    a.kdA  = afl(B_ * H_ * S_);
+    a.out  = (float*)d_out;
+
+    void* params[] = { &a };
+    hipLaunchCooperativeKernel((void*)mono, dim3(256), dim3(256), params, 0, stream);
+}
```
